# Optimization experiments

Hardware: AMD Instinct MI355X
Metric: run time of the kernel (lower is better)

Reference implementation:

```python
import jax, jax.numpy as jnp
import numpy as np

C = 64
B, H, W = 2, 128, 512
SCALE = C ** (-0.5)


def conv1x1(x, w, b):
    # x: [B,C,H,W], w: [O,I], b: [O]
    return jnp.einsum('bihw,oi->bohw', x, w) + b[None, :, None, None]


def dwconv3x3(x, w, b):
    # depthwise 3x3, w: [C,1,3,3]
    y = jax.lax.conv_general_dilated(
        x, w, window_strides=(1, 1), padding='SAME',
        feature_group_count=x.shape[1],
        dimension_numbers=('NCHW', 'OIHW', 'NCHW'))
    return y + b[None, :, None, None]


def proj12(x, w1, b1, wd, bd):
    return dwconv3x3(conv1x1(x, w1, b1), wd, bd)


def setup_inputs() -> dict:
    key = jax.random.key(0)
    ks = jax.random.split(key, 32)
    d = {}
    d['x_l'] = jax.random.normal(ks[0], (B, C, H, W), dtype=jnp.float32)
    d['x_r'] = jax.random.normal(ks[1], (B, C, H, W), dtype=jnp.float32)
    i = 2
    for p in ['lp1', 'rp1', 'lp2', 'rp2']:
        d[p + '_w1'] = jax.random.normal(ks[i], (C, C), dtype=jnp.float32) * 0.05; i += 1
        d[p + '_b1'] = jnp.zeros((C,), dtype=jnp.float32)
        d[p + '_wd'] = jax.random.normal(ks[i], (C, 1, 3, 3), dtype=jnp.float32) * 0.1; i += 1
        d[p + '_bd'] = jnp.zeros((C,), dtype=jnp.float32)
    for p in ['lp3', 'rp3']:
        d[p + '_w'] = jax.random.normal(ks[i], (C, C), dtype=jnp.float32) * 0.05; i += 1
        d[p + '_b'] = jnp.zeros((C,), dtype=jnp.float32)
    return d


def reference(x_l, x_r,
              lp1_w1, lp1_b1, lp1_wd, lp1_bd,
              rp1_w1, rp1_b1, rp1_wd, rp1_bd,
              lp2_w1, lp2_b1, lp2_wd, lp2_bd,
              rp2_w1, rp2_b1, rp2_wd, rp2_bd,
              lp3_w, lp3_b, rp3_w, rp3_b):
    Ql = proj12(x_l, lp1_w1, lp1_b1, lp1_wd, lp1_bd)  # [B,C,H,W]
    Qr = proj12(x_r, rp1_w1, rp1_b1, rp1_wd, rp1_bd)  # [B,C,H,W]
    # attention[b,h,w,v] = sum_c Ql[b,c,h,w] * Qr[b,c,h,v]
    att = jnp.einsum('bchw,bchv->bhwv', Ql, Qr) * SCALE  # [B,H,W,W]
    Vl = proj12(x_l, lp2_w1, lp2_b1, lp2_wd, lp2_bd)
    Vr = proj12(x_r, rp2_w1, rp2_b1, rp2_wd, rp2_bd)
    # softmax over right-view width (last axis), aggregate Vr
    A_r2l = jax.nn.softmax(att, axis=-1)
    F_r2l = jnp.einsum('bhwv,bchv->bchw', A_r2l, Vr)  # [B,C,H,W]
    # transposed attention, softmax over left-view width (axis -2 of att)
    A_l2r = jax.nn.softmax(att, axis=-2)
    F_l2r = jnp.einsum('bhwv,bchw->bchv', A_l2r, Vl)  # [B,C,H,W]
    F_r2l = conv1x1(F_r2l, lp3_w, lp3_b)
    F_l2r = conv1x1(F_l2r, rp3_w, rp3_b)
    return x_l + F_r2l + x_r + F_l2r
```

## Files before the change

### kernel.cpp

```cpp
#include <hip/hip_runtime.h>
#include <hip/hip_bf16.h>

typedef __attribute__((ext_vector_type(8))) short short8;
typedef __attribute__((ext_vector_type(4))) float f32x4;

#define QSCALE 0.18033688011112042f

__device__ __forceinline__ unsigned short f2bf(float f){
    unsigned u = __float_as_uint(f);
    unsigned r = (u + 0x7fffu + ((u>>16)&1u))>>16;
    return (unsigned short)r;
}
__device__ __forceinline__ unsigned pk_rtne(float hi, float lo){
    return (((unsigned)f2bf(hi))<<16) | (unsigned)f2bf(lo);
}

__global__ __launch_bounds__(256) void init_out_k(const float* __restrict__ xl,
                                                  const float* __restrict__ xr,
                                                  float* __restrict__ out, int n4){
    int i = blockIdx.x*256 + threadIdx.x;
    if (i < n4){
        const float4* a = (const float4*)xl;
        const float4* b = (const float4*)xr;
        float4 va = a[i], vb = b[i];
        float4 vo; vo.x=va.x+vb.x; vo.y=va.y+vb.y; vo.z=va.z+vb.z; vo.w=va.w+vb.w;
        ((float4*)out)[i] = vo;
    }
}

__global__ __launch_bounds__(256) void gemm_k(const float* __restrict__ x,
                                              const float* __restrict__ w1,
                                              const float* __restrict__ b1,
                                              unsigned short* __restrict__ T){
    __shared__ __align__(16) short sA[256*72];
    __shared__ __align__(16) short sB[64*72];
    __shared__ float sbias[64];
    int tid = threadIdx.x;
    int b = blockIdx.x >> 8;
    int hw0 = (blockIdx.x & 255) << 8;
    {
        int c = tid & 63, pq = tid >> 6;
        const float* xb = x + ((size_t)b<<22) + (size_t)c*65536 + hw0;
        #pragma unroll
        for (int it=0; it<16; it++){
            int piece = pq*16 + it;
            float4 v = *(const float4*)(xb + piece*4);
            int p = piece*4;
            sA[(p+0)*72 + c] = (short)f2bf(v.x);
            sA[(p+1)*72 + c] = (short)f2bf(v.y);
            sA[(p+2)*72 + c] = (short)f2bf(v.z);
            sA[(p+3)*72 + c] = (short)f2bf(v.w);
        }
        #pragma unroll
        for (int it=0; it<16; it++){
            int lin = it*256 + tid;
            int o = lin >> 6, cc = lin & 63;
            sB[o*72 + cc] = (short)f2bf(w1[lin]);
        }
        if (tid < 64) sbias[tid] = b1[tid];
    }
    __syncthreads();
    int wv = tid>>6, lane = tid&63, quad = lane>>4, l16 = lane&15;
    int m0 = wv*64;
    short8 a0[4], a1[4], bB0[4], bB1[4];
    #pragma unroll
    for (int mt=0; mt<4; mt++){
        a0[mt] = *(const short8*)(sA + (m0 + mt*16 + l16)*72 + quad*8);
        a1[mt] = *(const short8*)(sA + (m0 + mt*16 + l16)*72 + 32 + quad*8);
    }
    #pragma unroll
    for (int nt=0; nt<4; nt++){
        bB0[nt] = *(const short8*)(sB + (nt*16 + l16)*72 + quad*8);
        bB1[nt] = *(const short8*)(sB + (nt*16 + l16)*72 + 32 + quad*8);
    }
    const f32x4 z4 = {0.f,0.f,0.f,0.f};
    f32x4 acc[4][4];
    #pragma unroll
    for (int mt=0; mt<4; mt++)
        #pragma unroll
        for (int nt=0; nt<4; nt++){
            acc[mt][nt] = __builtin_amdgcn_mfma_f32_16x16x32_bf16(a0[mt], bB0[nt], z4, 0,0,0);
            acc[mt][nt] = __builtin_amdgcn_mfma_f32_16x16x32_bf16(a1[mt], bB1[nt], acc[mt][nt], 0,0,0);
        }
    int px0 = blockIdx.x << 8;
    #pragma unroll
    for (int nt=0; nt<4; nt++){
        float bias = sbias[nt*16 + l16];
        #pragma unroll
        for (int mt=0; mt<4; mt++){
            #pragma unroll
            for (int r=0;r<4;r++){
                int pxr = px0 + m0 + mt*16 + quad*4 + r;
                T[(size_t)pxr*64 + nt*16 + l16] = f2bf(acc[mt][nt][r] + bias);
            }
        }
    }
}

__global__ __launch_bounds__(256) void dwconv_k(const unsigned short* __restrict__ T,
                                                const float* __restrict__ wd,
                                                const float* __restrict__ bd,
                                                unsigned short* __restrict__ dst,
                                                int modeQ, float qscale){
    int bid = blockIdx.x;
    int wt = bid & 7, h = (bid>>3)&127, b = bid>>10;
    int tid = threadIdx.x;
    int cg = tid & 15, wl = tid >> 4;
    int c0 = cg*4;
    int w0 = wt*64 + wl*4;
    float acc[4][4];
    #pragma unroll
    for (int ch=0; ch<4; ch++){
        float bv = bd[c0+ch];
        #pragma unroll
        for (int i=0;i<4;i++) acc[ch][i] = bv;
    }
    const unsigned short* Tb = T + ((size_t)b<<22);
    #pragma unroll
    for (int dh=-1; dh<=1; dh++){
        int hh = h + dh;
        if (hh < 0 || hh > 127) continue;
        const unsigned short* Tr = Tb + ((size_t)(hh*512))*64 + c0;
        float win[6][4];
        #pragma unroll
        for (int j=0;j<6;j++){
            int ww = w0 - 1 + j;
            if (ww >= 0 && ww < 512){
                uint2 v = *(const uint2*)(Tr + (size_t)ww*64);
                win[j][0] = __uint_as_float(v.x<<16);
                win[j][1] = __uint_as_float(v.x & 0xffff0000u);
                win[j][2] = __uint_as_float(v.y<<16);
                win[j][3] = __uint_as_float(v.y & 0xffff0000u);
            } else {
                win[j][0]=0.f; win[j][1]=0.f; win[j][2]=0.f; win[j][3]=0.f;
            }
        }
        #pragma unroll
        for (int ch=0; ch<4; ch++){
            float k0 = wd[(c0+ch)*9 + (dh+1)*3];
            float k1 = wd[(c0+ch)*9 + (dh+1)*3 + 1];
            float k2 = wd[(c0+ch)*9 + (dh+1)*3 + 2];
            #pragma unroll
            for (int i=0;i<4;i++)
                acc[ch][i] += k0*win[i][ch] + k1*win[i+1][ch] + k2*win[i+2][ch];
        }
    }
    if (modeQ){
        int base = (b*128 + h)*512;
        #pragma unroll
        for (int i=0;i<4;i++){
            uint2 v;
            v.x = pk_rtne(acc[1][i]*qscale, acc[0][i]*qscale);
            v.y = pk_rtne(acc[3][i]*qscale, acc[2][i]*qscale);
            *(uint2*)(dst + ((size_t)(base + w0 + i))*64 + c0) = v;
        }
    } else {
        #pragma unroll
        for (int ch=0; ch<4; ch++){
            uint2 v;
            v.x = pk_rtne(acc[ch][1], acc[ch][0]);
            v.y = pk_rtne(acc[ch][3], acc[ch][2]);
            *(uint2*)(dst + (((size_t)(b*64 + c0 + ch))<<16) + h*512 + w0) = v;
        }
    }
}

#define PQ 72
#define PK 72
#define PV 72
#define PP 72
#define PW 72
#define PFA 72
#define POT 17
#define OFF_Q   0
#define OFF_K   9216
#define OFF_V   18432
#define OFF_W3  27648
#define LDS_TOT 36864

__global__ __launch_bounds__(256) void flash_k(
    const unsigned short* __restrict__ Ql, const unsigned short* __restrict__ Qr,
    const unsigned short* __restrict__ Vl, const unsigned short* __restrict__ Vr,
    const float* __restrict__ lw3, const float* __restrict__ lb3,
    const float* __restrict__ rw3, const float* __restrict__ rb3,
    float* __restrict__ out)
{
    __shared__ __align__(16) char smem[LDS_TOT];
    short* sQ  = (short*)(smem + OFF_Q);
    short* sK  = (short*)(smem + OFF_K);
    short* sV  = (short*)(smem + OFF_V);
    short* sP  = (short*)(smem + OFF_Q);
    short* sW  = (short*)(smem + OFF_W3);
    short* sFA = (short*)(smem + OFF_Q);
    float* sOT = (float*)(smem + OFF_K);

    int bid = blockIdx.x;
    int g  = ((bid >> 6) << 3) | (bid & 7);
    int qt = (bid >> 3) & 7;
    int h = g & 127, b = (g >> 7) & 1, dir = g >> 8;
    const unsigned short *Qg, *Kg, *Vg; const float *w3, *b3;
    if (dir==0){ Qg = Ql; Kg = Qr; Vg = Vr; w3 = lw3; b3 = lb3; }
    else       { Qg = Qr; Kg = Ql; Vg = Vl; w3 = rw3; b3 = rb3; }

    int tid = threadIdx.x;
    int wv = tid>>6, lane = tid&63, quad = lane>>4, l16 = lane&15;
    int bh = b*128 + h;

    {
        const uint4* src = (const uint4*)(Qg + ((size_t)bh*512 + qt*64)*64);
        #pragma unroll
        for (int it=0; it<2; it++){
            int idx = it*256 + tid;
            int row = idx>>3, piece = idx&7;
            *(uint4*)(sQ + row*PQ + piece*8) = src[idx];
        }
        #pragma unroll
        for (int it=0; it<16; it++){
            int idx = it*256 + tid;
            int o = idx>>6, cc = idx&63;
            sW[o*PW + cc] = (short)f2bf(w3[idx]);
        }
    }
    __syncthreads();

    short8 aq0 = *(const short8*)(sQ + (wv*16 + l16)*PQ + quad*8);
    short8 aq1 = *(const short8*)(sQ + (wv*16 + l16)*PQ + 32 + quad*8);

    const f32x4 z4 = {0.f,0.f,0.f,0.f};
    f32x4 oacc[4];
    #pragma unroll
    for (int ct=0; ct<4; ct++) oacc[ct] = z4;
    float lps = 0.f;

    const uint4* Ksrc = (const uint4*)(Kg + (size_t)bh*512*64);
    const unsigned short* Vbase = Vg + ((size_t)(b*64)*128 + h)*512;
    short* sPw = sP + wv*16*PP;

    for (int kt=0; kt<8; kt++){
        #pragma unroll
        for (int it=0; it<2; it++){
            int idx = it*256 + tid;
            int row = idx>>3, piece = idx&7;
            *(uint4*)(sK + row*PK + piece*8) = Ksrc[(size_t)(kt*64 + row)*8 + piece];
            uint4 vv = *(const uint4*)(Vbase + (size_t)row*65536 + kt*64 + piece*8);
            *(uint4*)(sV + row*PV + piece*8) = vv;
        }
        __syncthreads();
        #pragma unroll
        for (int nt=0; nt<4; nt++){
            short8 bk0 = *(const short8*)(sK + (nt*16 + l16)*PK + quad*8);
            short8 bk1 = *(const short8*)(sK + (nt*16 + l16)*PK + 32 + quad*8);
            f32x4 s = __builtin_amdgcn_mfma_f32_16x16x32_bf16(bk0, aq0, z4, 0,0,0);
            s       = __builtin_amdgcn_mfma_f32_16x16x32_bf16(bk1, aq1, s, 0,0,0);
            float p0 = __builtin_amdgcn_exp2f(s[0]);
            float p1 = __builtin_amdgcn_exp2f(s[1]);
            float p2 = __builtin_amdgcn_exp2f(s[2]);
            float p3 = __builtin_amdgcn_exp2f(s[3]);
            lps += (p0+p1) + (p2+p3);
            unsigned lo = __builtin_amdgcn_perm(__float_as_uint(p1), __float_as_uint(p0), 0x07060302);
            unsigned hi = __builtin_amdgcn_perm(__float_as_uint(p3), __float_as_uint(p2), 0x07060302);
            uint2 pv; pv.x = lo; pv.y = hi;
            *(uint2*)(sPw + l16*PP + nt*16 + quad*4) = pv;
        }
        short8 ap0 = *(const short8*)(sPw + l16*PP + quad*8);
        short8 ap1 = *(const short8*)(sPw + l16*PP + 32 + quad*8);
        #pragma unroll
        for (int ct=0; ct<4; ct++){
            short8 bv0 = *(const short8*)(sV + (ct*16 + l16)*PV + quad*8);
            short8 bv1 = *(const short8*)(sV + (ct*16 + l16)*PV + 32 + quad*8);
            oacc[ct] = __builtin_amdgcn_mfma_f32_16x16x32_bf16(ap0, bv0, oacc[ct], 0,0,0);
            oacc[ct] = __builtin_amdgcn_mfma_f32_16x16x32_bf16(ap1, bv1, oacc[ct], 0,0,0);
        }
        __syncthreads();
    }

    float l = lps;
    l += __shfl_xor(l, 16);
    l += __shfl_xor(l, 32);
    float inv[4];
    #pragma unroll
    for (int r=0;r<4;r++) inv[r] = 1.0f / __shfl(l, quad*4 + r);

    short* sFw = sFA + wv*16*PFA;
    #pragma unroll
    for (int ct=0; ct<4; ct++){
        #pragma unroll
        for (int r=0;r<4;r++)
            sFw[(quad*4+r)*PFA + ct*16 + l16] = (short)f2bf(oacc[ct][r]*inv[r]);
    }
    short8 af0 = *(const short8*)(sFw + l16*PFA + quad*8);
    short8 af1 = *(const short8*)(sFw + l16*PFA + 32 + quad*8);
    f32x4 d2[4];
    #pragma unroll
    for (int ot=0; ot<4; ot++){
        short8 bw0 = *(const short8*)(sW + (ot*16 + l16)*PW + quad*8);
        short8 bw1 = *(const short8*)(sW + (ot*16 + l16)*PW + 32 + quad*8);
        d2[ot] = __builtin_amdgcn_mfma_f32_16x16x32_bf16(af0, bw0, z4, 0,0,0);
        d2[ot] = __builtin_amdgcn_mfma_f32_16x16x32_bf16(af1, bw1, d2[ot], 0,0,0);
        float bias = b3[ot*16 + l16];
        #pragma unroll
        for (int r=0;r<4;r++) d2[ot][r] += bias;
    }
    __syncthreads();
    float* sOw = sOT + wv*(64*POT);
    #pragma unroll
    for (int ot=0; ot<4; ot++){
        #pragma unroll
        for (int r=0;r<4;r++)
            sOw[(ot*16 + l16)*POT + quad*4 + r] = d2[ot][r];
    }
    int wbase = qt*64 + wv*16;
    #pragma unroll
    for (int it=0; it<16; it++){
        int o = it*4 + quad;
        float val = sOw[o*POT + l16];
        unsafeAtomicAdd(out + ((size_t)(b*64 + o)*128 + h)*512 + wbase + l16, val);
    }
}

extern "C" void kernel_launch(void* const* d_in, const int* in_sizes, int n_in,
                              void* d_out, int out_size, void* d_ws, size_t ws_size,
                              hipStream_t stream)
{
    const float* xl = (const float*)d_in[0];
    const float* xr = (const float*)d_in[1];
    const float* lp1_w1 = (const float*)d_in[2];
    const float* lp1_b1 = (const float*)d_in[3];
    const float* lp1_wd = (const float*)d_in[4];
    const float* lp1_bd = (const float*)d_in[5];
    const float* rp1_w1 = (const float*)d_in[6];
    const float* rp1_b1 = (const float*)d_in[7];
    const float* rp1_wd = (const float*)d_in[8];
    const float* rp1_bd = (const float*)d_in[9];
    const float* lp2_w1 = (const float*)d_in[10];
    const float* lp2_b1 = (const float*)d_in[11];
    const float* lp2_wd = (const float*)d_in[12];
    const float* lp2_bd = (const float*)d_in[13];
    const float* rp2_w1 = (const float*)d_in[14];
    const float* rp2_b1 = (const float*)d_in[15];
    const float* rp2_wd = (const float*)d_in[16];
    const float* rp2_bd = (const float*)d_in[17];
    const float* lp3_w  = (const float*)d_in[18];
    const float* lp3_b  = (const float*)d_in[19];
    const float* rp3_w  = (const float*)d_in[20];
    const float* rp3_b  = (const float*)d_in[21];
    float* out = (float*)d_out;

    const size_t S = 16777216;
    char* ws = (char*)d_ws;
    unsigned short* T   = (unsigned short*)(ws);
    unsigned short* Ql  = (unsigned short*)(ws + 1*S);
    unsigned short* Qr  = (unsigned short*)(ws + 2*S);
    unsigned short* Vl  = (unsigned short*)(ws + 3*S);
    unsigned short* Vr  = (unsigned short*)(ws + 4*S);

    init_out_k<<<8192, 256, 0, stream>>>(xl, xr, out, 2097152);

    gemm_k<<<512, 256, 0, stream>>>(xl, lp1_w1, lp1_b1, T);
    dwconv_k<<<2048, 256, 0, stream>>>(T, lp1_wd, lp1_bd, Ql, 1, QSCALE);
    gemm_k<<<512, 256, 0, stream>>>(xl, lp2_w1, lp2_b1, T);
    dwconv_k<<<2048, 256, 0, stream>>>(T, lp2_wd, lp2_bd, Vl, 0, 1.0f);

    gemm_k<<<512, 256, 0, stream>>>(xr, rp1_w1, rp1_b1, T);
    dwconv_k<<<2048, 256, 0, stream>>>(T, rp1_wd, rp1_bd, Qr, 1, 1.0f);
    gemm_k<<<512, 256, 0, stream>>>(xr, rp2_w1, rp2_b1, T);
    dwconv_k<<<2048, 256, 0, stream>>>(T, rp2_wd, rp2_bd, Vr, 0, 1.0f);

    flash_k<<<4096, 256, 0, stream>>>(Ql, Qr, Vl, Vr, lp3_w, lp3_b, rp3_w, rp3_b, out);
}
```

Measured before the change: 340.1 us.

## Fuse projection preprocessing: transpose inputs once, pair Q/V gemms and dwconvs

After: 328.1 us. 3.5% less time.

```diff
diff --git a/kernel.cpp b/kernel.cpp
--- a/kernel.cpp
+++ b/kernel.cpp
@@ -15,107 +15,152 @@
     return (((unsigned)f2bf(hi))<<16) | (unsigned)f2bf(lo);
 }
 
-__global__ __launch_bounds__(256) void init_out_k(const float* __restrict__ xl,
-                                                  const float* __restrict__ xr,
-                                                  float* __restrict__ out, int n4){
-    int i = blockIdx.x*256 + threadIdx.x;
-    if (i < n4){
-        const float4* a = (const float4*)xl;
-        const float4* b = (const float4*)xr;
-        float4 va = a[i], vb = b[i];
+__global__ __launch_bounds__(256) void prep_k(const float* __restrict__ xl,
+                                              const float* __restrict__ xr,
+                                              float* __restrict__ out,
+                                              unsigned short* __restrict__ XtL,
+                                              unsigned short* __restrict__ XtR){
+    __shared__ float ft[64*65];
+    int bid = blockIdx.x;
+    int strip = bid & 1023, b = bid >> 10;
+    int px0 = strip << 6;
+    int tid = threadIdx.x;
+    float4 vrs[4];
+    #pragma unroll
+    for (int it=0; it<4; it++){
+        int lin = it*256 + tid;
+        int c = lin >> 4, piece = lin & 15;
+        size_t off = (((size_t)(b*64 + c))<<16) + px0 + piece*4;
+        float4 va = *(const float4*)(xl + off);
+        float4 vb = *(const float4*)(xr + off);
+        vrs[it] = vb;
         float4 vo; vo.x=va.x+vb.x; vo.y=va.y+vb.y; vo.z=va.z+vb.z; vo.w=va.w+vb.w;
-        ((float4*)out)[i] = vo;
-    }
-}
-
-__global__ __launch_bounds__(256) void gemm_k(const float* __restrict__ x,
-                                              const float* __restrict__ w1,
-                                              const float* __restrict__ b1,
-                                              unsigned short* __restrict__ T){
+        *(float4*)(out + off) = vo;
+        float* d = ft + c*65 + piece*4;
+        d[0]=va.x; d[1]=va.y; d[2]=va.z; d[3]=va.w;
+    }
+    __syncthreads();
+    #pragma unroll
+    for (int it=0; it<2; it++){
+        int lin = it*256 + tid;
+        int pxl = lin >> 3, cb = lin & 7;
+        unsigned r[4];
+        #pragma unroll
+        for (int j=0;j<4;j++){
+            unsigned lo = f2bf(ft[(cb*8 + 2*j  )*65 + pxl]);
+            unsigned hi = f2bf(ft[(cb*8 + 2*j+1)*65 + pxl]);
+            r[j] = lo | (hi<<16);
+        }
+        uint4 v; v.x=r[0]; v.y=r[1]; v.z=r[2]; v.w=r[3];
+        *(uint4*)(XtL + ((size_t)(b<<16) + px0 + pxl)*64 + cb*8) = v;
+    }
+    __syncthreads();
+    #pragma unroll
+    for (int it=0; it<4; it++){
+        int lin = it*256 + tid;
+        int c = lin >> 4, piece = lin & 15;
+        float4 vb = vrs[it];
+        float* d = ft + c*65 + piece*4;
+        d[0]=vb.x; d[1]=vb.y; d[2]=vb.z; d[3]=vb.w;
+    }
+    __syncthreads();
+    #pragma unroll
+    for (int it=0; it<2; it++){
+        int lin = it*256 + tid;
+        int pxl = lin >> 3, cb = lin & 7;
+        unsigned r[4];
+        #pragma unroll
+        for (int j=0;j<4;j++){
+            unsigned lo = f2bf(ft[(cb*8 + 2*j  )*65 + pxl]);
+            unsigned hi = f2bf(ft[(cb*8 + 2*j+1)*65 + pxl]);
+            r[j] = lo | (hi<<16);
+        }
+        uint4 v; v.x=r[0]; v.y=r[1]; v.z=r[2]; v.w=r[3];
+        *(uint4*)(XtR + ((size_t)(b<<16) + px0 + pxl)*64 + cb*8) = v;
+    }
+}
+
+__global__ __launch_bounds__(256) void gemm_k(const unsigned short* __restrict__ Xt,
+                                              const float* __restrict__ wA,
+                                              const float* __restrict__ bA,
+                                              const float* __restrict__ wB,
+                                              const float* __restrict__ bB,
+                                              unsigned short* __restrict__ T1,
+                                              unsigned short* __restrict__ T2){
     __shared__ __align__(16) short sA[256*72];
-    __shared__ __align__(16) short sB[64*72];
-    __shared__ float sbias[64];
+    __shared__ __align__(16) short sB[128*72];
+    __shared__ float sbias[128];
     int tid = threadIdx.x;
-    int b = blockIdx.x >> 8;
-    int hw0 = (blockIdx.x & 255) << 8;
+    int px0 = blockIdx.x << 8;
     {
-        int c = tid & 63, pq = tid >> 6;
-        const float* xb = x + ((size_t)b<<22) + (size_t)c*65536 + hw0;
-        #pragma unroll
-        for (int it=0; it<16; it++){
-            int piece = pq*16 + it;
-            float4 v = *(const float4*)(xb + piece*4);
-            int p = piece*4;
-            sA[(p+0)*72 + c] = (short)f2bf(v.x);
-            sA[(p+1)*72 + c] = (short)f2bf(v.y);
-            sA[(p+2)*72 + c] = (short)f2bf(v.z);
-            sA[(p+3)*72 + c] = (short)f2bf(v.w);
-        }
-        #pragma unroll
-        for (int it=0; it<16; it++){
+        const uint4* src = (const uint4*)(Xt + (size_t)px0*64);
+        #pragma unroll
+        for (int it=0; it<8; it++){
+            int lin = it*256 + tid;
+            int row = lin >> 3, piece = lin & 7;
+            *(uint4*)(sA + row*72 + piece*8) = src[lin];
+        }
+        #pragma unroll
+        for (int it=0; it<32; it++){
             int lin = it*256 + tid;
             int o = lin >> 6, cc = lin & 63;
-            sB[o*72 + cc] = (short)f2bf(w1[lin]);
-        }
-        if (tid < 64) sbias[tid] = b1[tid];
+            float wv = (o < 64) ? wA[o*64 + cc] : wB[(o-64)*64 + cc];
+            sB[o*72 + cc] = (short)f2bf(wv);
+        }
+        if (tid < 128) sbias[tid] = (tid < 64) ? bA[tid] : bB[tid-64];
     }
     __syncthreads();
     int wv = tid>>6, lane = tid&63, quad = lane>>4, l16 = lane&15;
     int m0 = wv*64;
-    short8 a0[4], a1[4], bB0[4], bB1[4];
+    short8 a0[4], a1[4];
     #pragma unroll
     for (int mt=0; mt<4; mt++){
         a0[mt] = *(const short8*)(sA + (m0 + mt*16 + l16)*72 + quad*8);
         a1[mt] = *(const short8*)(sA + (m0 + mt*16 + l16)*72 + 32 + quad*8);
     }
-    #pragma unroll
-    for (int nt=0; nt<4; nt++){
-        bB0[nt] = *(const short8*)(sB + (nt*16 + l16)*72 + quad*8);
-        bB1[nt] = *(const short8*)(sB + (nt*16 + l16)*72 + 32 + quad*8);
-    }
     const f32x4 z4 = {0.f,0.f,0.f,0.f};
-    f32x4 acc[4][4];
-    #pragma unroll
-    for (int mt=0; mt<4; mt++)
+    #pragma unroll
+    for (int set=0; set<2; set++){
+        unsigned short* T = set ? T2 : T1;
+        short8 bB0[4], bB1[4];
         #pragma unroll
         for (int nt=0; nt<4; nt++){
-            acc[mt][nt] = __builtin_amdgcn_mfma_f32_16x16x32_bf16(a0[mt], bB0[nt], z4, 0,0,0);
-            acc[mt][nt] = __builtin_amdgcn_mfma_f32_16x16x32_bf16(a1[mt], bB1[nt], acc[mt][nt], 0,0,0);
-        }
-    int px0 = blockIdx.x << 8;
-    #pragma unroll
-    for (int nt=0; nt<4; nt++){
-        float bias = sbias[nt*16 + l16];
-        #pragma unroll
-        for (int mt=0; mt<4; mt++){
+            bB0[nt] = *(const short8*)(sB + (set*64 + nt*16 + l16)*72 + quad*8);
+            bB1[nt] = *(const short8*)(sB + (set*64 + nt*16 + l16)*72 + 32 + quad*8);
+        }
+        f32x4 acc[4][4];
+        #pragma unroll
+        for (int mt=0; mt<4; mt++)
             #pragma unroll
-            for (int r=0;r<4;r++){
-                int pxr = px0 + m0 + mt*16 + quad*4 + r;
-                T[(size_t)pxr*64 + nt*16 + l16] = f2bf(acc[mt][nt][r] + bias);
+            for (int nt=0; nt<4; nt++){
+                acc[mt][nt] = __builtin_amdgcn_mfma_f32_16x16x32_bf16(a0[mt], bB0[nt], z4, 0,0,0);
+                acc[mt][nt] = __builtin_amdgcn_mfma_f32_16x16x32_bf16(a1[mt], bB1[nt], acc[mt][nt], 0,0,0);
             }
-        }
-    }
-}
-
-__global__ __launch_bounds__(256) void dwconv_k(const unsigned short* __restrict__ T,
-                                                const float* __restrict__ wd,
-                                                const float* __restrict__ bd,
-                                                unsigned short* __restrict__ dst,
-                                                int modeQ, float qscale){
-    int bid = blockIdx.x;
-    int wt = bid & 7, h = (bid>>3)&127, b = bid>>10;
-    int tid = threadIdx.x;
-    int cg = tid & 15, wl = tid >> 4;
-    int c0 = cg*4;
-    int w0 = wt*64 + wl*4;
-    float acc[4][4];
+        #pragma unroll
+        for (int nt=0; nt<4; nt++){
+            float bias = sbias[set*64 + nt*16 + l16];
+            #pragma unroll
+            for (int mt=0; mt<4; mt++){
+                #pragma unroll
+                for (int r=0;r<4;r++){
+                    int pxr = px0 + m0 + mt*16 + quad*4 + r;
+                    T[(size_t)pxr*64 + nt*16 + l16] = f2bf(acc[mt][nt][r] + bias);
+                }
+            }
+        }
+    }
+}
+
+__device__ __forceinline__ void dw_tile(const unsigned short* __restrict__ Tb,
+                                        const float* __restrict__ wd,
+                                        const float* __restrict__ bd,
+                                        int c0, int w0, int h, float acc[4][4]){
     #pragma unroll
     for (int ch=0; ch<4; ch++){
         float bv = bd[c0+ch];
         #pragma unroll
         for (int i=0;i<4;i++) acc[ch][i] = bv;
     }
-    const unsigned short* Tb = T + ((size_t)b<<22);
     #pragma unroll
     for (int dh=-1; dh<=1; dh++){
         int hh = h + dh;
@@ -145,22 +190,43 @@
                 acc[ch][i] += k0*win[i][ch] + k1*win[i+1][ch] + k2*win[i+2][ch];
         }
     }
-    if (modeQ){
+}
+
+__global__ __launch_bounds__(256) void dwconv_k(const unsigned short* __restrict__ T1,
+                                                const unsigned short* __restrict__ T2,
+                                                const float* __restrict__ wd1,
+                                                const float* __restrict__ bd1,
+                                                const float* __restrict__ wd2,
+                                                const float* __restrict__ bd2,
+                                                unsigned short* __restrict__ Qdst,
+                                                unsigned short* __restrict__ Vdst,
+                                                float qscale){
+    int bid = blockIdx.x;
+    int wt = bid & 7, h = (bid>>3)&127, b = bid>>10;
+    int tid = threadIdx.x;
+    int cg = tid & 15, wl = tid >> 4;
+    int c0 = cg*4;
+    int w0 = wt*64 + wl*4;
+    float acc[4][4];
+    dw_tile(T1 + ((size_t)b<<22), wd1, bd1, c0, w0, h, acc);
+    {
         int base = (b*128 + h)*512;
         #pragma unroll
         for (int i=0;i<4;i++){
             uint2 v;
             v.x = pk_rtne(acc[1][i]*qscale, acc[0][i]*qscale);
             v.y = pk_rtne(acc[3][i]*qscale, acc[2][i]*qscale);
-            *(uint2*)(dst + ((size_t)(base + w0 + i))*64 + c0) = v;
-        }
-    } else {
+            *(uint2*)(Qdst + ((size_t)(base + w0 + i))*64 + c0) = v;
+        }
+    }
+    dw_tile(T2 + ((size_t)b<<22), wd2, bd2, c0, w0, h, acc);
+    {
         #pragma unroll
         for (int ch=0; ch<4; ch++){
             uint2 v;
             v.x = pk_rtne(acc[ch][1], acc[ch][0]);
             v.y = pk_rtne(acc[ch][3], acc[ch][2]);
-            *(uint2*)(dst + (((size_t)(b*64 + c0 + ch))<<16) + h*512 + w0) = v;
+            *(uint2*)(Vdst + (((size_t)(b*64 + c0 + ch))<<16) + h*512 + w0) = v;
         }
     }
 }
@@ -348,23 +414,22 @@
 
     const size_t S = 16777216;
     char* ws = (char*)d_ws;
-    unsigned short* T   = (unsigned short*)(ws);
-    unsigned short* Ql  = (unsigned short*)(ws + 1*S);
-    unsigned short* Qr  = (unsigned short*)(ws + 2*S);
-    unsigned short* Vl  = (unsigned short*)(ws + 3*S);
-    unsigned short* Vr  = (unsigned short*)(ws + 4*S);
-
-    init_out_k<<<8192, 256, 0, stream>>>(xl, xr, out, 2097152);
-
-    gemm_k<<<512, 256, 0, stream>>>(xl, lp1_w1, lp1_b1, T);
-    dwconv_k<<<2048, 256, 0, stream>>>(T, lp1_wd, lp1_bd, Ql, 1, QSCALE);
-    gemm_k<<<512, 256, 0, stream>>>(xl, lp2_w1, lp2_b1, T);
-    dwconv_k<<<2048, 256, 0, stream>>>(T, lp2_wd, lp2_bd, Vl, 0, 1.0f);
-
-    gemm_k<<<512, 256, 0, stream>>>(xr, rp1_w1, rp1_b1, T);
-    dwconv_k<<<2048, 256, 0, stream>>>(T, rp1_wd, rp1_bd, Qr, 1, 1.0f);
-    gemm_k<<<512, 256, 0, stream>>>(xr, rp2_w1, rp2_b1, T);
-    dwconv_k<<<2048, 256, 0, stream>>>(T, rp2_wd, rp2_bd, Vr, 0, 1.0f);
+    unsigned short* T1  = (unsigned short*)(ws);
+    unsigned short* T2  = (unsigned short*)(ws + 1*S);
+    unsigned short* Ql  = (unsigned short*)(ws + 2*S);
+    unsigned short* Qr  = (unsigned short*)(ws + 3*S);
+    unsigned short* Vl  = (unsigned short*)(ws + 4*S);
+    unsigned short* Vr  = (unsigned short*)(ws + 5*S);
+    unsigned short* XtL = Qr;
+    unsigned short* XtR = Vr;
+
+    prep_k<<<2048, 256, 0, stream>>>(xl, xr, out, XtL, XtR);
+
+    gemm_k<<<512, 256, 0, stream>>>(XtL, lp1_w1, lp1_b1, lp2_w1, lp2_b1, T1, T2);
+    dwconv_k<<<2048, 256, 0, stream>>>(T1, T2, lp1_wd, lp1_bd, lp2_wd, lp2_bd, Ql, Vl, QSCALE);
+
+    gemm_k<<<512, 256, 0, stream>>>(XtR, rp1_w1, rp1_b1, rp2_w1, rp2_b1, T1, T2);
+    dwconv_k<<<2048, 256, 0, stream>>>(T1, T2, rp1_wd, rp1_bd, rp2_wd, rp2_bd, Qr, Vr, 1.0f);
 
     flash_k<<<4096, 256, 0, stream>>>(Ql, Qr, Vl, Vr, lp3_w, lp3_b, rp3_w, rp3_b, out);
 }
```

## Fuse 1x1 conv GEMM and depthwise conv into one projection kernel

Applied to the files above, without the earlier changes.

Result: slower. 361.9 us (+6.4%).

```diff
diff --git a/kernel.cpp b/kernel.cpp
--- a/kernel.cpp
+++ b/kernel.cpp
@@ -28,139 +28,144 @@
     }
 }
 
-__global__ __launch_bounds__(256) void gemm_k(const float* __restrict__ x,
-                                              const float* __restrict__ w1,
-                                              const float* __restrict__ b1,
-                                              unsigned short* __restrict__ T){
-    __shared__ __align__(16) short sA[256*72];
-    __shared__ __align__(16) short sB[64*72];
-    __shared__ float sbias[64];
-    int tid = threadIdx.x;
-    int b = blockIdx.x >> 8;
-    int hw0 = (blockIdx.x & 255) << 8;
-    {
-        int c = tid & 63, pq = tid >> 6;
-        const float* xb = x + ((size_t)b<<22) + (size_t)c*65536 + hw0;
-        #pragma unroll
-        for (int it=0; it<16; it++){
-            int piece = pq*16 + it;
-            float4 v = *(const float4*)(xb + piece*4);
-            int p = piece*4;
-            sA[(p+0)*72 + c] = (short)f2bf(v.x);
-            sA[(p+1)*72 + c] = (short)f2bf(v.y);
-            sA[(p+2)*72 + c] = (short)f2bf(v.z);
-            sA[(p+3)*72 + c] = (short)f2bf(v.w);
-        }
-        #pragma unroll
-        for (int it=0; it<16; it++){
-            int lin = it*256 + tid;
-            int o = lin >> 6, cc = lin & 63;
-            sB[o*72 + cc] = (short)f2bf(w1[lin]);
-        }
-        if (tid < 64) sbias[tid] = b1[tid];
-    }
-    __syncthreads();
-    int wv = tid>>6, lane = tid&63, quad = lane>>4, l16 = lane&15;
-    int m0 = wv*64;
-    short8 a0[4], a1[4], bB0[4], bB1[4];
-    #pragma unroll
-    for (int mt=0; mt<4; mt++){
-        a0[mt] = *(const short8*)(sA + (m0 + mt*16 + l16)*72 + quad*8);
-        a1[mt] = *(const short8*)(sA + (m0 + mt*16 + l16)*72 + 32 + quad*8);
-    }
-    #pragma unroll
-    for (int nt=0; nt<4; nt++){
-        bB0[nt] = *(const short8*)(sB + (nt*16 + l16)*72 + quad*8);
-        bB1[nt] = *(const short8*)(sB + (nt*16 + l16)*72 + 32 + quad*8);
-    }
-    const f32x4 z4 = {0.f,0.f,0.f,0.f};
-    f32x4 acc[4][4];
-    #pragma unroll
-    for (int mt=0; mt<4; mt++)
-        #pragma unroll
-        for (int nt=0; nt<4; nt++){
-            acc[mt][nt] = __builtin_amdgcn_mfma_f32_16x16x32_bf16(a0[mt], bB0[nt], z4, 0,0,0);
-            acc[mt][nt] = __builtin_amdgcn_mfma_f32_16x16x32_bf16(a1[mt], bB1[nt], acc[mt][nt], 0,0,0);
-        }
-    int px0 = blockIdx.x << 8;
-    #pragma unroll
-    for (int nt=0; nt<4; nt++){
-        float bias = sbias[nt*16 + l16];
-        #pragma unroll
-        for (int mt=0; mt<4; mt++){
-            #pragma unroll
-            for (int r=0;r<4;r++){
-                int pxr = px0 + m0 + mt*16 + quad*4 + r;
-                T[(size_t)pxr*64 + nt*16 + l16] = f2bf(acc[mt][nt][r] + bias);
-            }
-        }
-    }
-}
-
-__global__ __launch_bounds__(256) void dwconv_k(const unsigned short* __restrict__ T,
-                                                const float* __restrict__ wd,
-                                                const float* __restrict__ bd,
-                                                unsigned short* __restrict__ dst,
-                                                int modeQ, float qscale){
+#define FM 208
+__global__ __launch_bounds__(256) void fused_proj_k(
+    const float* __restrict__ x,
+    const float* __restrict__ w1, const float* __restrict__ b1,
+    const float* __restrict__ wd1, const float* __restrict__ bd1,
+    const float* __restrict__ w2, const float* __restrict__ b2,
+    const float* __restrict__ wd2, const float* __restrict__ bd2,
+    unsigned short* __restrict__ Qdst, unsigned short* __restrict__ Vdst,
+    float qscale)
+{
+    __shared__ __align__(16) short sA[FM*72];
+    __shared__ __align__(16) short sT[FM*72];
     int bid = blockIdx.x;
     int wt = bid & 7, h = (bid>>3)&127, b = bid>>10;
     int tid = threadIdx.x;
+    int w0 = wt << 6;
+
+    if (tid < 192){
+        int c = tid & 63, hr = tid >> 6;
+        int hh = h - 1 + hr;
+        int hc = min(max(hh, 0), 127);
+        const float* xrow = x + ((size_t)(b*64 + c)*128 + hc)*512;
+        short* dst = sA + (hr*66)*72 + c;
+        {
+            int wc = max(w0 - 1, 0);
+            dst[0] = (short)f2bf(xrow[wc]);
+        }
+        #pragma unroll
+        for (int j=0; j<16; j++){
+            float4 v = *(const float4*)(xrow + w0 + j*4);
+            int wi = 1 + j*4;
+            dst[(wi+0)*72] = (short)f2bf(v.x);
+            dst[(wi+1)*72] = (short)f2bf(v.y);
+            dst[(wi+2)*72] = (short)f2bf(v.z);
+            dst[(wi+3)*72] = (short)f2bf(v.w);
+        }
+        {
+            int wc = min(w0 + 64, 511);
+            dst[65*72] = (short)f2bf(xrow[wc]);
+        }
+    }
+    __syncthreads();
+
+    int wv = tid>>6, lane = tid&63, quad = lane>>4, l16 = lane&15;
     int cg = tid & 15, wl = tid >> 4;
     int c0 = cg*4;
-    int w0 = wt*64 + wl*4;
-    float acc[4][4];
-    #pragma unroll
-    for (int ch=0; ch<4; ch++){
-        float bv = bd[c0+ch];
-        #pragma unroll
-        for (int i=0;i<4;i++) acc[ch][i] = bv;
-    }
-    const unsigned short* Tb = T + ((size_t)b<<22);
-    #pragma unroll
-    for (int dh=-1; dh<=1; dh++){
-        int hh = h + dh;
-        if (hh < 0 || hh > 127) continue;
-        const unsigned short* Tr = Tb + ((size_t)(hh*512))*64 + c0;
-        float win[6][4];
-        #pragma unroll
-        for (int j=0;j<6;j++){
-            int ww = w0 - 1 + j;
-            if (ww >= 0 && ww < 512){
-                uint2 v = *(const uint2*)(Tr + (size_t)ww*64);
-                win[j][0] = __uint_as_float(v.x<<16);
-                win[j][1] = __uint_as_float(v.x & 0xffff0000u);
-                win[j][2] = __uint_as_float(v.y<<16);
-                win[j][3] = __uint_as_float(v.y & 0xffff0000u);
-            } else {
-                win[j][0]=0.f; win[j][1]=0.f; win[j][2]=0.f; win[j][3]=0.f;
-            }
-        }
+    const f32x4 z4 = {0.f,0.f,0.f,0.f};
+
+    for (int set=0; set<2; set++){
+        const float* wset = set ? w2 : w1;
+        const float* bset = set ? b2 : b1;
+        short8 bw0[4], bw1[4]; float bias[4];
+        #pragma unroll
+        for (int nt=0; nt<4; nt++){
+            const float* wrow = wset + (nt*16 + l16)*64 + quad*8;
+            float4 wa = *(const float4*)(wrow);
+            float4 wb = *(const float4*)(wrow + 4);
+            float4 wc = *(const float4*)(wrow + 32);
+            float4 we = *(const float4*)(wrow + 36);
+            bw0[nt][0]=(short)f2bf(wa.x); bw0[nt][1]=(short)f2bf(wa.y); bw0[nt][2]=(short)f2bf(wa.z); bw0[nt][3]=(short)f2bf(wa.w);
+            bw0[nt][4]=(short)f2bf(wb.x); bw0[nt][5]=(short)f2bf(wb.y); bw0[nt][6]=(short)f2bf(wb.z); bw0[nt][7]=(short)f2bf(wb.w);
+            bw1[nt][0]=(short)f2bf(wc.x); bw1[nt][1]=(short)f2bf(wc.y); bw1[nt][2]=(short)f2bf(wc.z); bw1[nt][3]=(short)f2bf(wc.w);
+            bw1[nt][4]=(short)f2bf(we.x); bw1[nt][5]=(short)f2bf(we.y); bw1[nt][6]=(short)f2bf(we.z); bw1[nt][7]=(short)f2bf(we.w);
+            bias[nt] = bset[nt*16 + l16];
+        }
+        for (int mt = wv; mt < 13; mt += 4){
+            short8 a0 = *(const short8*)(sA + (mt*16 + l16)*72 + quad*8);
+            short8 a1 = *(const short8*)(sA + (mt*16 + l16)*72 + 32 + quad*8);
+            f32x4 acc[4];
+            #pragma unroll
+            for (int nt=0; nt<4; nt++){
+                acc[nt] = __builtin_amdgcn_mfma_f32_16x16x32_bf16(a0, bw0[nt], z4, 0,0,0);
+                acc[nt] = __builtin_amdgcn_mfma_f32_16x16x32_bf16(a1, bw1[nt], acc[nt], 0,0,0);
+            }
+            #pragma unroll
+            for (int nt=0; nt<4; nt++){
+                #pragma unroll
+                for (int r=0;r<4;r++)
+                    sT[(mt*16 + quad*4 + r)*72 + nt*16 + l16] = (short)f2bf(acc[nt][r] + bias[nt]);
+            }
+        }
+        __syncthreads();
+        const float* wdk = set ? wd2 : wd1;
+        const float* bdk = set ? bd2 : bd1;
+        float acc[4][4];
         #pragma unroll
         for (int ch=0; ch<4; ch++){
-            float k0 = wd[(c0+ch)*9 + (dh+1)*3];
-            float k1 = wd[(c0+ch)*9 + (dh+1)*3 + 1];
-            float k2 = wd[(c0+ch)*9 + (dh+1)*3 + 2];
-            #pragma unroll
-            for (int i=0;i<4;i++)
-                acc[ch][i] += k0*win[i][ch] + k1*win[i+1][ch] + k2*win[i+2][ch];
-        }
-    }
-    if (modeQ){
-        int base = (b*128 + h)*512;
-        #pragma unroll
-        for (int i=0;i<4;i++){
-            uint2 v;
-            v.x = pk_rtne(acc[1][i]*qscale, acc[0][i]*qscale);
-            v.y = pk_rtne(acc[3][i]*qscale, acc[2][i]*qscale);
-            *(uint2*)(dst + ((size_t)(base + w0 + i))*64 + c0) = v;
-        }
-    } else {
-        #pragma unroll
-        for (int ch=0; ch<4; ch++){
-            uint2 v;
-            v.x = pk_rtne(acc[ch][1], acc[ch][0]);
-            v.y = pk_rtne(acc[ch][3], acc[ch][2]);
-            *(uint2*)(dst + (((size_t)(b*64 + c0 + ch))<<16) + h*512 + w0) = v;
+            float bv = bdk[c0+ch];
+            #pragma unroll
+            for (int i=0;i<4;i++) acc[ch][i] = bv;
+        }
+        #pragma unroll
+        for (int dh=-1; dh<=1; dh++){
+            int hh = h + dh;
+            if (hh < 0 || hh > 127) continue;
+            const short* Trow = sT + ((dh+1)*66)*72 + c0;
+            float win[6][4];
+            #pragma unroll
+            for (int j=0;j<6;j++){
+                int wimg = w0 - 1 + wl*4 + j;
+                if (wimg >= 0 && wimg < 512){
+                    uint2 v = *(const uint2*)(Trow + (wl*4 + j)*72);
+                    win[j][0] = __uint_as_float(v.x<<16);
+                    win[j][1] = __uint_as_float(v.x & 0xffff0000u);
+                    win[j][2] = __uint_as_float(v.y<<16);
+                    win[j][3] = __uint_as_float(v.y & 0xffff0000u);
+                } else {
+                    win[j][0]=0.f; win[j][1]=0.f; win[j][2]=0.f; win[j][3]=0.f;
+                }
+            }
+            #pragma unroll
+            for (int ch=0; ch<4; ch++){
+                float k0 = wdk[(c0+ch)*9 + (dh+1)*3];
+                float k1 = wdk[(c0+ch)*9 + (dh+1)*3 + 1];
+                float k2 = wdk[(c0+ch)*9 + (dh+1)*3 + 2];
+                #pragma unroll
+                for (int i=0;i<4;i++)
+                    acc[ch][i] += k0*win[i][ch] + k1*win[i+1][ch] + k2*win[i+2][ch];
+            }
+        }
+        if (set == 0){
+            int base = (b*128 + h)*512;
+            #pragma unroll
+            for (int i=0;i<4;i++){
+                uint2 v;
+                v.x = pk_rtne(acc[1][i]*qscale, acc[0][i]*qscale);
+                v.y = pk_rtne(acc[3][i]*qscale, acc[2][i]*qscale);
+                *(uint2*)(Qdst + ((size_t)(base + w0 + wl*4 + i))*64 + c0) = v;
+            }
+            __syncthreads();
+        } else {
+            #pragma unroll
+            for (int ch=0; ch<4; ch++){
+                uint2 v;
+                v.x = pk_rtne(acc[ch][1], acc[ch][0]);
+                v.y = pk_rtne(acc[ch][3], acc[ch][2]);
+                *(uint2*)(Vdst + (((size_t)(b*64 + c0 + ch))<<16) + h*512 + w0 + wl*4) = v;
+            }
         }
     }
 }
@@ -348,23 +353,22 @@
 
     const size_t S = 16777216;
     char* ws = (char*)d_ws;
-    unsigned short* T   = (unsigned short*)(ws);
-    unsigned short* Ql  = (unsigned short*)(ws + 1*S);
-    unsigned short* Qr  = (unsigned short*)(ws + 2*S);
-    unsigned short* Vl  = (unsigned short*)(ws + 3*S);
-    unsigned short* Vr  = (unsigned short*)(ws + 4*S);
+    unsigned short* Ql  = (unsigned short*)(ws);
+    unsigned short* Qr  = (unsigned short*)(ws + 1*S);
+    unsigned short* Vl  = (unsigned short*)(ws + 2*S);
+    unsigned short* Vr  = (unsigned short*)(ws + 3*S);
 
     init_out_k<<<8192, 256, 0, stream>>>(xl, xr, out, 2097152);
 
-    gemm_k<<<512, 256, 0, stream>>>(xl, lp1_w1, lp1_b1, T);
-    dwconv_k<<<2048, 256, 0, stream>>>(T, lp1_wd, lp1_bd, Ql, 1, QSCALE);
-    gemm_k<<<512, 256, 0, stream>>>(xl, lp2_w1, lp2_b1, T);
-    dwconv_k<<<2048, 256, 0, stream>>>(T, lp2_wd, lp2_bd, Vl, 0, 1.0f);
-
-    gemm_k<<<512, 256, 0, stream>>>(xr, rp1_w1, rp1_b1, T);
-    dwconv_k<<<2048, 256, 0, stream>>>(T, rp1_wd, rp1_bd, Qr, 1, 1.0f);
-    gemm_k<<<512, 256, 0, stream>>>(xr, rp2_w1, rp2_b1, T);
-    dwconv_k<<<2048, 256, 0, stream>>>(T, rp2_wd, rp2_bd, Vr, 0, 1.0f);
+    fused_proj_k<<<2048, 256, 0, stream>>>(xl,
+        lp1_w1, lp1_b1, lp1_wd, lp1_bd,
+        lp2_w1, lp2_b1, lp2_wd, lp2_bd,
+        Ql, Vl, QSCALE);
+
+    fused_proj_k<<<2048, 256, 0, stream>>>(xr,
+        rp1_w1, rp1_b1, rp1_wd, rp1_bd,
+        rp2_w1, rp2_b1, rp2_wd, rp2_bd,
+        Qr, Vr, 1.0f);
 
     flash_k<<<4096, 256, 0, stream>>>(Ql, Qr, Vl, Vr, lp3_w, lp3_b, rp3_w, rp3_b, out);
 }
```
